# Kernel optimization log

Measured on AMD Instinct MI355X. Metric: run time of the kernel, lower is better.

## Reference

```python
import jax, jax.numpy as jnp
import numpy as np

EMBED_DIM = 1024
NUM_HEADS = 16
RANK = 32
HEAD_DIM = EMBED_DIM // NUM_HEADS
SCALE = 1.0 / np.sqrt(RANK).astype(np.float32)


def setup_inputs() -> dict:
    key = jax.random.key(0)
    ks = jax.random.split(key, 9)
    B, S = 2, 2048
    def lin(k, fan_in, fan_out):
        bound = 1.0 / np.sqrt(fan_in)
        return jax.random.uniform(k, (fan_in, fan_out), jnp.float32, -bound, bound)
    return {
        "hidden_states": jax.random.normal(ks[0], (B, S, EMBED_DIM), jnp.float32),
        "Wq": lin(ks[1], EMBED_DIM, RANK * NUM_HEADS),
        "bq": jnp.zeros((RANK * NUM_HEADS,), jnp.float32),
        "Wk": lin(ks[2], EMBED_DIM, RANK * NUM_HEADS),
        "bk": jnp.zeros((RANK * NUM_HEADS,), jnp.float32),
        "Wv": lin(ks[3], EMBED_DIM, EMBED_DIM),
        "bv": jnp.zeros((EMBED_DIM,), jnp.float32),
        "Wo": lin(ks[4], EMBED_DIM, EMBED_DIM),
        "bo": jnp.zeros((EMBED_DIM,), jnp.float32),
    }


def reference(hidden_states, Wq, bq, Wk, bk, Wv, bv, Wo, bo):
    B, S, E = hidden_states.shape
    q = (hidden_states @ Wq + bq).reshape(B, S, NUM_HEADS, RANK)      # [b,i,h,r]
    k = (hidden_states @ Wk + bk).reshape(B, S, NUM_HEADS, RANK)      # [b,j,h,r]
    v = (hidden_states @ Wv + bv).reshape(B, S, NUM_HEADS, HEAD_DIM)  # [b,j,h,d]
    # full [b,i,j,h] score tensor, softmax over j (axis=2), as in the torch code
    scores = jnp.einsum('bihr,bjhr->bijh', q, k) * SCALE
    attn = jax.nn.softmax(scores, axis=2)
    out = jnp.einsum('bijh,bjhd->bihd', attn, v).reshape(B, S, E)
    return out @ Wo + bo
```

## Files before the change

kernel.cpp:

```cpp
#include <hip/hip_runtime.h>

#define EMBED   1024
#define NHEADS  16
#define RANK    32
#define HDIM    64
#define BATCH   2
#define SEQ     2048
#define BSQ     (BATCH * SEQ)
#define CEXP    0.25505998f

typedef __attribute__((ext_vector_type(8))) short bf16x8;
typedef __attribute__((ext_vector_type(4))) float f32x4;

__device__ __forceinline__ float bf2f(unsigned short u) {
    union { unsigned int i; float f; } x; x.i = ((unsigned int)u) << 16;
    return x.f;
}
__device__ __forceinline__ unsigned short f2bf(float f) {
    union { float f; unsigned int i; } x; x.f = f;
    unsigned int r = x.i + 0x7FFFu + ((x.i >> 16) & 1u);
    return (unsigned short)(r >> 16);
}

#define ASYNC16(gp, lp) \
    __builtin_amdgcn_global_load_lds( \
        (const __attribute__((address_space(1))) void*)(gp), \
        (__attribute__((address_space(3))) void*)(lp), 16, 0, 0)

__global__ __launch_bounds__(256) void prep_all(
    const float* __restrict__ hs,
    const float* __restrict__ Wq, const float* __restrict__ Wk,
    const float* __restrict__ Wv, const float* __restrict__ Wo,
    const float* __restrict__ bq, const float* __restrict__ bk,
    const float* __restrict__ bv,
    unsigned short* __restrict__ hsb, unsigned short* __restrict__ wT_all,
    unsigned short* __restrict__ woT, float* __restrict__ ball)
{
    __shared__ float L[64][65];
    const int blk = blockIdx.x;
    const int t = threadIdx.x;

    if (blk < 2048) {
        const size_t i = ((size_t)blk * 256 + t) * 8;
        float4 v0 = *(const float4*)(hs + i);
        float4 v1 = *(const float4*)(hs + i + 4);
        ushort4 o0, o1;
        o0.x = f2bf(v0.x); o0.y = f2bf(v0.y); o0.z = f2bf(v0.z); o0.w = f2bf(v0.w);
        o1.x = f2bf(v1.x); o1.y = f2bf(v1.y); o1.z = f2bf(v1.z); o1.w = f2bf(v1.w);
        *(ushort4*)(hsb + i) = o0;
        *(ushort4*)(hsb + i + 4) = o1;
        return;
    }
    if (blk < 2816) {
        int idx = blk - 2048;
        int z, bx, by;
        if (idx < 256) { z = idx >> 7; int r2 = idx & 127; bx = r2 & 7; by = r2 >> 3; }
        else { idx -= 256; z = 2 + (idx >> 8); int r2 = idx & 255; bx = r2 & 15; by = r2 >> 4; }
        const int Nw = (z < 2) ? 512 : 1024;
        const float* W = (z == 0) ? Wq : (z == 1) ? Wk : (z == 2) ? Wv : Wo;
        unsigned short* dst = (z == 3) ? woT : (wT_all + (size_t)z * 512 * 1024);

        const int r = t >> 2, c0 = (t & 3) * 16;
        const float* src = W + (size_t)(by * 64 + r) * Nw + bx * 64 + c0;
        #pragma unroll
        for (int u = 0; u < 4; u++)
            *(float4*)&L[r][c0 + 4 * u] = *(const float4*)(src + 4 * u);
        __syncthreads();
        unsigned short* drow = dst + (size_t)(bx * 64 + r) * 1024 + by * 64 + c0;
        #pragma unroll
        for (int u4 = 0; u4 < 4; u4++) {
            ushort4 o;
            o.x = f2bf(L[c0 + 4 * u4 + 0][r]);
            o.y = f2bf(L[c0 + 4 * u4 + 1][r]);
            o.z = f2bf(L[c0 + 4 * u4 + 2][r]);
            o.w = f2bf(L[c0 + 4 * u4 + 3][r]);
            *(ushort4*)(drow + 4 * u4) = o;
        }
        return;
    }
    {
        const int i = (blk - 2816) * 256 + t;
        ball[i] = (i < 512) ? bq[i] : (i < 1024) ? bk[i - 512] : bv[i - 1024];
    }
}

__global__ __launch_bounds__(256) void gemm_qkv(
    const unsigned short* __restrict__ A, const unsigned short* __restrict__ BT,
    const float* __restrict__ bias,
    unsigned short* __restrict__ qH, unsigned short* __restrict__ kH,
    unsigned short* __restrict__ vTout)
{
    __shared__ unsigned short As[128 * 32];
    __shared__ unsigned short Bs[64 * 32];
    const int K = 1024;
    const int t = threadIdx.x;
    const int lane = t & 63;
    const int li = lane & 15, la = lane >> 4;
    const int w = t >> 6;
    const int row0 = blockIdx.y * 128, col0 = blockIdx.x * 64;

    const int sr = lane >> 2, sc2 = (lane & 3) * 8;
    const unsigned short* ag0 = A + (size_t)(row0 + w * 32 + sr) * K + sc2;
    const unsigned short* ag1 = A + (size_t)(row0 + w * 32 + 16 + sr) * K + sc2;
    const unsigned short* bg0 = BT + (size_t)(col0 + w * 16 + sr) * K + sc2;
    unsigned short* lA0 = &As[(w * 32) * 32];
    unsigned short* lA1 = &As[(w * 32 + 16) * 32];
    unsigned short* lB0 = &Bs[(w * 16) * 32];

    f32x4 acc[2][4];
    #pragma unroll
    for (int i = 0; i < 2; i++)
        #pragma unroll
        for (int j = 0; j < 4; j++)
            acc[i][j] = (f32x4){0.f, 0.f, 0.f, 0.f};

    for (int k0 = 0; k0 < K; k0 += 32) {
        ASYNC16(ag0 + k0, lA0);
        ASYNC16(ag1 + k0, lA1);
        ASYNC16(bg0 + k0, lB0);
        __syncthreads();
        bf16x8 af[2], bfr[4];
        #pragma unroll
        for (int mt = 0; mt < 2; mt++)
            af[mt] = *(const bf16x8*)&As[(w * 32 + mt * 16 + li) * 32 + la * 8];
        #pragma unroll
        for (int nt = 0; nt < 4; nt++)
            bfr[nt] = *(const bf16x8*)&Bs[(nt * 16 + li) * 32 + la * 8];
        #pragma unroll
        for (int mt = 0; mt < 2; mt++)
            #pragma unroll
            for (int nt = 0; nt < 4; nt++)
                acc[mt][nt] = __builtin_amdgcn_mfma_f32_16x16x32_bf16(af[mt], bfr[nt], acc[mt][nt], 0, 0, 0);
        __syncthreads();
    }

    const int bb = row0 >> 11;
    const int jb = (row0 & 2047) + w * 32;
    #pragma unroll
    for (int nt = 0; nt < 4; nt++) {
        const int col = col0 + nt * 16 + li;
        const float bval = bias[col];
        if (col < 1024) {
            const int hh = (col & 511) >> 5;
            const int rr = col & 31;
            unsigned short* base = ((col < 512) ? qH : kH)
                + ((size_t)(bb * 16 + hh) * 2048) * 32 + rr;
            #pragma unroll
            for (int mt = 0; mt < 2; mt++)
                #pragma unroll
                for (int r = 0; r < 4; r++)
                    base[(size_t)(jb + mt * 16 + la * 4 + r) * 32] =
                        f2bf(acc[mt][nt][r] + bval);
        } else {
            const int hd = col - 1024;
            unsigned short* dcol = vTout + ((size_t)(bb * 16 + (hd >> 6)) * 64 + (hd & 63)) * SEQ;
            #pragma unroll
            for (int mt = 0; mt < 2; mt++) {
                const int srow = jb + mt * 16 + la * 4;
                ushort4 o;
                o.x = f2bf(acc[mt][nt][0] + bval);
                o.y = f2bf(acc[mt][nt][1] + bval);
                o.z = f2bf(acc[mt][nt][2] + bval);
                o.w = f2bf(acc[mt][nt][3] + bval);
                *(ushort4*)(dcol + srow) = o;
            }
        }
    }
}

__global__ __launch_bounds__(256) void gemm_out(
    const unsigned short* __restrict__ A, const unsigned short* __restrict__ BT,
    const float* __restrict__ bias, float* __restrict__ C)
{
    __shared__ unsigned short As[64 * 32];
    __shared__ unsigned short Bs[64 * 32];
    const int K = 1024;
    const int t = threadIdx.x;
    const int lane = t & 63;
    const int li = lane & 15, la = lane >> 4;
    const int w = t >> 6;
    const int row0 = blockIdx.y * 64, col0 = blockIdx.x * 64;

    const int sr = lane >> 2, sc2 = (lane & 3) * 8;
    const unsigned short* ag0 = A + (size_t)(row0 + w * 16 + sr) * K + sc2;
    const unsigned short* bg0 = BT + (size_t)(col0 + w * 16 + sr) * K + sc2;
    unsigned short* lA0 = &As[(w * 16) * 32];
    unsigned short* lB0 = &Bs[(w * 16) * 32];

    f32x4 acc[4];
    #pragma unroll
    for (int j = 0; j < 4; j++) acc[j] = (f32x4){0.f, 0.f, 0.f, 0.f};

    for (int k0 = 0; k0 < K; k0 += 32) {
        ASYNC16(ag0 + k0, lA0);
        ASYNC16(bg0 + k0, lB0);
        __syncthreads();
        bf16x8 af, bfr[4];
        af = *(const bf16x8*)&As[(w * 16 + li) * 32 + la * 8];
        #pragma unroll
        for (int nt = 0; nt < 4; nt++)
            bfr[nt] = *(const bf16x8*)&Bs[(nt * 16 + li) * 32 + la * 8];
        #pragma unroll
        for (int nt = 0; nt < 4; nt++)
            acc[nt] = __builtin_amdgcn_mfma_f32_16x16x32_bf16(af, bfr[nt], acc[nt], 0, 0, 0);
        __syncthreads();
    }

    #pragma unroll
    for (int nt = 0; nt < 4; nt++) {
        const int col = col0 + nt * 16 + li;
        const float bval = bias[col];
        #pragma unroll
        for (int r = 0; r < 4; r++) {
            const int row = row0 + w * 16 + la * 4 + r;
            C[(size_t)row * 1024 + col] = acc[nt][r] + bval;
        }
    }
}

__global__ __launch_bounds__(256) void attn_v7(
    const unsigned short* __restrict__ qH,
    const unsigned short* __restrict__ kH,
    const unsigned short* __restrict__ vT,
    unsigned short* __restrict__ ao)
{
    __shared__ unsigned short kt[2][64 * 48];
    __shared__ unsigned short vt[2][64 * 72];
    __shared__ unsigned short P[128 * 72];

    const int t = threadIdx.x;
    const int lane = t & 63;
    const int li = lane & 15, la = lane >> 4;
    const int w = t >> 6;

    const int bh = blockIdx.x & 31;
    const int itile = blockIdx.x >> 5;
    const int i0 = itile * 128;
    const int b = bh >> 4, h = bh & 15;

    bf16x8 qf[2];
    #pragma unroll
    for (int it = 0; it < 2; it++) {
        const unsigned short* qp = qH + ((size_t)bh * 2048 + i0 + w * 32 + it * 16 + li) * 32 + la * 8;
        ushort4 q0 = *(const ushort4*)qp;
        ushort4 q1 = *(const ushort4*)(qp + 4);
        short u[8];
        u[0] = (short)f2bf(bf2f(q0.x) * CEXP);
        u[1] = (short)f2bf(bf2f(q0.y) * CEXP);
        u[2] = (short)f2bf(bf2f(q0.z) * CEXP);
        u[3] = (short)f2bf(bf2f(q0.w) * CEXP);
        u[4] = (short)f2bf(bf2f(q1.x) * CEXP);
        u[5] = (short)f2bf(bf2f(q1.y) * CEXP);
        u[6] = (short)f2bf(bf2f(q1.z) * CEXP);
        u[7] = (short)f2bf(bf2f(q1.w) * CEXP);
        qf[it] = *(const bf16x8*)u;
    }

    bf16x8 vones;
    #pragma unroll
    for (int u2 = 0; u2 < 8; u2++) vones[u2] = (short)0x3F80;

    const int kr = t >> 2, kc = (t & 3) * 8;
    const int vr = t >> 3, vc = (t & 7) * 8;
    const unsigned short* kp = kH + (size_t)bh * 2048 * 32 + (size_t)kr * 32 + kc;
    const unsigned short* vp0 = vT + (size_t)bh * 64 * SEQ + (size_t)vr * SEQ + vc;
    const unsigned short* vp1 = vp0 + (size_t)32 * SEQ;

    f32x4 accO[2][4], accl[2];
    #pragma unroll
    for (int mt = 0; mt < 2; mt++) {
        accl[mt] = (f32x4){0.f, 0.f, 0.f, 0.f};
        #pragma unroll
        for (int dt = 0; dt < 4; dt++) accO[mt][dt] = (f32x4){0.f, 0.f, 0.f, 0.f};
    }

    uint4 kreg  = *(const uint4*)(kp);
    uint4 vreg0 = *(const uint4*)(vp0);
    uint4 vreg1 = *(const uint4*)(vp1);
    *(uint4*)&kt[0][kr * 48 + kc] = kreg;
    *(uint4*)&vt[0][vr * 72 + vc] = vreg0;
    *(uint4*)&vt[0][(vr + 32) * 72 + vc] = vreg1;
    kreg  = *(const uint4*)(kp + 64 * 32);
    vreg0 = *(const uint4*)(vp0 + 64);
    vreg1 = *(const uint4*)(vp1 + 64);

    #define ATTN_BODY(BUF, OTHER, JPRE)                                            \
    {                                                                              \
        __syncthreads();                                                           \
        *(uint4*)&kt[OTHER][kr * 48 + kc] = kreg;                                  \
        *(uint4*)&vt[OTHER][vr * 72 + vc] = vreg0;                                 \
        *(uint4*)&vt[OTHER][(vr + 32) * 72 + vc] = vreg1;                          \
        const int jn = (JPRE) & 2047;                                              \
        kreg  = *(const uint4*)(kp + (size_t)jn * 32);                             \
        vreg0 = *(const uint4*)(vp0 + jn);                                         \
        vreg1 = *(const uint4*)(vp1 + jn);                                         \
        f32x4 sc[4][2];                                                            \
        _Pragma("unroll")                                                          \
        for (int jt = 0; jt < 4; jt++) {                                           \
            const bf16x8 kf = *(const bf16x8*)&kt[BUF][(jt * 16 + li) * 48 + la * 8]; \
            sc[jt][0] = __builtin_amdgcn_mfma_f32_16x16x32_bf16(kf, qf[0], (f32x4){0.f,0.f,0.f,0.f}, 0, 0, 0); \
            sc[jt][1] = __builtin_amdgcn_mfma_f32_16x16x32_bf16(kf, qf[1], (f32x4){0.f,0.f,0.f,0.f}, 0, 0, 0); \
        }                                                                          \
        _Pragma("unroll")                                                          \
        for (int jt = 0; jt < 4; jt++)                                             \
            _Pragma("unroll")                                                      \
            for (int it = 0; it < 2; it++) {                                       \
                union { float f; unsigned int u; } c0, c1, c2, c3;                 \
                c0.f = exp2f(sc[jt][it][0]);                                       \
                c1.f = exp2f(sc[jt][it][1]);                                       \
                c2.f = exp2f(sc[jt][it][2]);                                       \
                c3.f = exp2f(sc[jt][it][3]);                                       \
                uint2 pk;                                                          \
                pk.x = __builtin_amdgcn_perm(c1.u + 0x8000u, c0.u + 0x8000u, 0x07060302u); \
                pk.y = __builtin_amdgcn_perm(c3.u + 0x8000u, c2.u + 0x8000u, 0x07060302u); \
                *(uint2*)&P[(w * 32 + it * 16 + li) * 72 + jt * 16 + la * 4] = pk; \
            }                                                                      \
        _Pragma("unroll")                                                          \
        for (int mt = 0; mt < 2; mt++) {                                           \
            _Pragma("unroll")                                                      \
            for (int ks = 0; ks < 2; ks++) {                                       \
                const bf16x8 pf = *(const bf16x8*)&P[(w * 32 + mt * 16 + li) * 72 + ks * 32 + la * 8]; \
                accl[mt] = __builtin_amdgcn_mfma_f32_16x16x32_bf16(pf, vones, accl[mt], 0, 0, 0); \
                _Pragma("unroll")                                                  \
                for (int dt = 0; dt < 4; dt++) {                                   \
                    const bf16x8 vf = *(const bf16x8*)&vt[BUF][(dt * 16 + li) * 72 + ks * 32 + la * 8]; \
                    accO[mt][dt] = __builtin_amdgcn_mfma_f32_16x16x32_bf16(pf, vf, accO[mt][dt], 0, 0, 0); \
                }                                                                  \
            }                                                                      \
        }                                                                          \
    }

    for (int j0 = 0; j0 < SEQ; j0 += 128) {
        ATTN_BODY(0, 1, j0 + 128)
        ATTN_BODY(1, 0, j0 + 192)
    }
    #undef ATTN_BODY

    #pragma unroll
    for (int mt = 0; mt < 2; mt++) {
        float linv[4];
        #pragma unroll
        for (int r = 0; r < 4; r++) linv[r] = 1.f / accl[mt][r];
        #pragma unroll
        for (int dt = 0; dt < 4; dt++)
            #pragma unroll
            for (int r = 0; r < 4; r++) {
                const int row = b * SEQ + i0 + w * 32 + mt * 16 + la * 4 + r;
                ao[(size_t)row * 1024 + h * 64 + dt * 16 + li] = f2bf(accO[mt][dt][r] * linv[r]);
            }
    }
}

extern "C" void kernel_launch(void* const* d_in, const int* in_sizes, int n_in,
                              void* d_out, int out_size, void* d_ws, size_t ws_size,
                              hipStream_t stream) {
    const float* hs = (const float*)d_in[0];
    const float* Wq = (const float*)d_in[1];
    const float* bq = (const float*)d_in[2];
    const float* Wk = (const float*)d_in[3];
    const float* bk = (const float*)d_in[4];
    const float* Wv = (const float*)d_in[5];
    const float* bv = (const float*)d_in[6];
    const float* Wo = (const float*)d_in[7];
    const float* bo = (const float*)d_in[8];

    char* p = (char*)d_ws;
    unsigned short* hsb = (unsigned short*)(p);
    unsigned short* wT  = (unsigned short*)(p + 8388608u);
    unsigned short* woT = (unsigned short*)(p + 12582912u);
    float*          ball= (float*)(p + 14680064u);
    unsigned short* qHb = (unsigned short*)(p + 14688256u);
    unsigned short* kHb = (unsigned short*)(p + 18882560u);
    unsigned short* vTb = (unsigned short*)(p + 23076864u);
    unsigned short* ao  = (unsigned short*)(p + 31465472u);

    prep_all<<<dim3(2824), 256, 0, stream>>>(hs, Wq, Wk, Wv, Wo, bq, bk, bv,
                                             hsb, wT, woT, ball);

    gemm_qkv<<<dim3(32, 32), 256, 0, stream>>>(hsb, wT, ball, qHb, kHb, vTb);

    attn_v7<<<dim3(512), 256, 0, stream>>>(qHb, kHb, vTb, ao);

    gemm_out<<<dim3(16, 64), 256, 0, stream>>>(ao, woT, bo, (float*)d_out);
}
```

Before: 196.2 us.

## Retile QKV and output GEMMs to larger tiles, halve attention query tile

The QKV GEMM moves to 128x128 tiles and the output GEMM to 64x128 tiles, each with a 2x2 warp layout and a 64-wide K step per barrier pair. This raises data reuse per load and halves the number of barriers. The attention kernel drops to 64 query rows per block (16 per warp) and doubles the grid to 1024 blocks, trading per-block K/V reuse for more parallelism and fewer registers. The new GEMM grids have fewer blocks, which may underfill the 256 CUs.

```diff
diff --git a/kernel.cpp b/kernel.cpp
--- a/kernel.cpp
+++ b/kernel.cpp
@@ -90,55 +90,59 @@
     unsigned short* __restrict__ qH, unsigned short* __restrict__ kH,
     unsigned short* __restrict__ vTout)
 {
-    __shared__ unsigned short As[128 * 32];
-    __shared__ unsigned short Bs[64 * 32];
+    __shared__ unsigned short As[2 * 128 * 32];
+    __shared__ unsigned short Bs[2 * 128 * 32];
     const int K = 1024;
     const int t = threadIdx.x;
     const int lane = t & 63;
     const int li = lane & 15, la = lane >> 4;
-    const int w = t >> 6;
-    const int row0 = blockIdx.y * 128, col0 = blockIdx.x * 64;
+    const int w = t >> 6, wm = w >> 1, wn = w & 1;
+    const int row0 = blockIdx.y * 128, col0 = blockIdx.x * 128;
 
     const int sr = lane >> 2, sc2 = (lane & 3) * 8;
-    const unsigned short* ag0 = A + (size_t)(row0 + w * 32 + sr) * K + sc2;
-    const unsigned short* ag1 = A + (size_t)(row0 + w * 32 + 16 + sr) * K + sc2;
-    const unsigned short* bg0 = BT + (size_t)(col0 + w * 16 + sr) * K + sc2;
-    unsigned short* lA0 = &As[(w * 32) * 32];
-    unsigned short* lA1 = &As[(w * 32 + 16) * 32];
-    unsigned short* lB0 = &Bs[(w * 16) * 32];
-
-    f32x4 acc[2][4];
-    #pragma unroll
-    for (int i = 0; i < 2; i++)
+    const unsigned short* ag = A + (size_t)(row0 + sr) * K + sc2;
+    const unsigned short* bg = BT + (size_t)(col0 + sr) * K + sc2;
+
+    f32x4 acc[4][4];
+    #pragma unroll
+    for (int i = 0; i < 4; i++)
         #pragma unroll
         for (int j = 0; j < 4; j++)
             acc[i][j] = (f32x4){0.f, 0.f, 0.f, 0.f};
 
-    for (int k0 = 0; k0 < K; k0 += 32) {
-        ASYNC16(ag0 + k0, lA0);
-        ASYNC16(ag1 + k0, lA1);
-        ASYNC16(bg0 + k0, lB0);
-        __syncthreads();
-        bf16x8 af[2], bfr[4];
-        #pragma unroll
-        for (int mt = 0; mt < 2; mt++)
-            af[mt] = *(const bf16x8*)&As[(w * 32 + mt * 16 + li) * 32 + la * 8];
-        #pragma unroll
-        for (int nt = 0; nt < 4; nt++)
-            bfr[nt] = *(const bf16x8*)&Bs[(nt * 16 + li) * 32 + la * 8];
-        #pragma unroll
-        for (int mt = 0; mt < 2; mt++)
+    for (int k0 = 0; k0 < K; k0 += 64) {
+        #pragma unroll
+        for (int kh = 0; kh < 2; kh++)
+            #pragma unroll
+            for (int u = 0; u < 2; u++) {
+                const int ro = w * 32 + u * 16;
+                ASYNC16(ag + (size_t)ro * K + k0 + kh * 32, &As[kh * 4096 + ro * 32]);
+                ASYNC16(bg + (size_t)ro * K + k0 + kh * 32, &Bs[kh * 4096 + ro * 32]);
+            }
+        __syncthreads();
+        #pragma unroll
+        for (int kh = 0; kh < 2; kh++) {
+            bf16x8 af[4], bfr[4];
+            #pragma unroll
+            for (int mt = 0; mt < 4; mt++)
+                af[mt] = *(const bf16x8*)&As[kh * 4096 + (wm * 64 + mt * 16 + li) * 32 + la * 8];
             #pragma unroll
             for (int nt = 0; nt < 4; nt++)
-                acc[mt][nt] = __builtin_amdgcn_mfma_f32_16x16x32_bf16(af[mt], bfr[nt], acc[mt][nt], 0, 0, 0);
+                bfr[nt] = *(const bf16x8*)&Bs[kh * 4096 + (wn * 64 + nt * 16 + li) * 32 + la * 8];
+            #pragma unroll
+            for (int mt = 0; mt < 4; mt++)
+                #pragma unroll
+                for (int nt = 0; nt < 4; nt++)
+                    acc[mt][nt] = __builtin_amdgcn_mfma_f32_16x16x32_bf16(af[mt], bfr[nt], acc[mt][nt], 0, 0, 0);
+        }
         __syncthreads();
     }
 
     const int bb = row0 >> 11;
-    const int jb = (row0 & 2047) + w * 32;
+    const int jb = (row0 & 2047) + wm * 64;
     #pragma unroll
     for (int nt = 0; nt < 4; nt++) {
-        const int col = col0 + nt * 16 + li;
+        const int col = col0 + wn * 64 + nt * 16 + li;
         const float bval = bias[col];
         if (col < 1024) {
             const int hh = (col & 511) >> 5;
@@ -146,7 +150,7 @@
             unsigned short* base = ((col < 512) ? qH : kH)
                 + ((size_t)(bb * 16 + hh) * 2048) * 32 + rr;
             #pragma unroll
-            for (int mt = 0; mt < 2; mt++)
+            for (int mt = 0; mt < 4; mt++)
                 #pragma unroll
                 for (int r = 0; r < 4; r++)
                     base[(size_t)(jb + mt * 16 + la * 4 + r) * 32] =
@@ -155,7 +159,7 @@
             const int hd = col - 1024;
             unsigned short* dcol = vTout + ((size_t)(bb * 16 + (hd >> 6)) * 64 + (hd & 63)) * SEQ;
             #pragma unroll
-            for (int mt = 0; mt < 2; mt++) {
+            for (int mt = 0; mt < 4; mt++) {
                 const int srow = jb + mt * 16 + la * 4;
                 ushort4 o;
                 o.x = f2bf(acc[mt][nt][0] + bval);
@@ -172,53 +176,70 @@
     const unsigned short* __restrict__ A, const unsigned short* __restrict__ BT,
     const float* __restrict__ bias, float* __restrict__ C)
 {
-    __shared__ unsigned short As[64 * 32];
-    __shared__ unsigned short Bs[64 * 32];
+    __shared__ unsigned short As[2 * 64 * 32];
+    __shared__ unsigned short Bs[2 * 128 * 32];
     const int K = 1024;
     const int t = threadIdx.x;
     const int lane = t & 63;
     const int li = lane & 15, la = lane >> 4;
-    const int w = t >> 6;
-    const int row0 = blockIdx.y * 64, col0 = blockIdx.x * 64;
+    const int w = t >> 6, wm = w >> 1, wn = w & 1;
+    const int row0 = blockIdx.y * 64, col0 = blockIdx.x * 128;
 
     const int sr = lane >> 2, sc2 = (lane & 3) * 8;
-    const unsigned short* ag0 = A + (size_t)(row0 + w * 16 + sr) * K + sc2;
-    const unsigned short* bg0 = BT + (size_t)(col0 + w * 16 + sr) * K + sc2;
-    unsigned short* lA0 = &As[(w * 16) * 32];
-    unsigned short* lB0 = &Bs[(w * 16) * 32];
-
-    f32x4 acc[4];
-    #pragma unroll
-    for (int j = 0; j < 4; j++) acc[j] = (f32x4){0.f, 0.f, 0.f, 0.f};
-
-    for (int k0 = 0; k0 < K; k0 += 32) {
-        ASYNC16(ag0 + k0, lA0);
-        ASYNC16(bg0 + k0, lB0);
-        __syncthreads();
-        bf16x8 af, bfr[4];
-        af = *(const bf16x8*)&As[(w * 16 + li) * 32 + la * 8];
-        #pragma unroll
-        for (int nt = 0; nt < 4; nt++)
-            bfr[nt] = *(const bf16x8*)&Bs[(nt * 16 + li) * 32 + la * 8];
-        #pragma unroll
-        for (int nt = 0; nt < 4; nt++)
-            acc[nt] = __builtin_amdgcn_mfma_f32_16x16x32_bf16(af, bfr[nt], acc[nt], 0, 0, 0);
+    const unsigned short* ag = A + (size_t)(row0 + sr) * K + sc2;
+    const unsigned short* bg = BT + (size_t)(col0 + sr) * K + sc2;
+
+    f32x4 acc[2][4];
+    #pragma unroll
+    for (int i = 0; i < 2; i++)
+        #pragma unroll
+        for (int j = 0; j < 4; j++)
+            acc[i][j] = (f32x4){0.f, 0.f, 0.f, 0.f};
+
+    for (int k0 = 0; k0 < K; k0 += 64) {
+        #pragma unroll
+        for (int kh = 0; kh < 2; kh++) {
+            ASYNC16(ag + (size_t)(w * 16) * K + k0 + kh * 32, &As[kh * 2048 + (w * 16) * 32]);
+            #pragma unroll
+            for (int u = 0; u < 2; u++) {
+                const int ro = w * 32 + u * 16;
+                ASYNC16(bg + (size_t)ro * K + k0 + kh * 32, &Bs[kh * 4096 + ro * 32]);
+            }
+        }
+        __syncthreads();
+        #pragma unroll
+        for (int kh = 0; kh < 2; kh++) {
+            bf16x8 af[2], bfr[4];
+            #pragma unroll
+            for (int mt = 0; mt < 2; mt++)
+                af[mt] = *(const bf16x8*)&As[kh * 2048 + (wm * 32 + mt * 16 + li) * 32 + la * 8];
+            #pragma unroll
+            for (int nt = 0; nt < 4; nt++)
+                bfr[nt] = *(const bf16x8*)&Bs[kh * 4096 + (wn * 64 + nt * 16 + li) * 32 + la * 8];
+            #pragma unroll
+            for (int mt = 0; mt < 2; mt++)
+                #pragma unroll
+                for (int nt = 0; nt < 4; nt++)
+                    acc[mt][nt] = __builtin_amdgcn_mfma_f32_16x16x32_bf16(af[mt], bfr[nt], acc[mt][nt], 0, 0, 0);
+        }
         __syncthreads();
     }
 
     #pragma unroll
     for (int nt = 0; nt < 4; nt++) {
-        const int col = col0 + nt * 16 + li;
+        const int col = col0 + wn * 64 + nt * 16 + li;
         const float bval = bias[col];
         #pragma unroll
-        for (int r = 0; r < 4; r++) {
-            const int row = row0 + w * 16 + la * 4 + r;
-            C[(size_t)row * 1024 + col] = acc[nt][r] + bval;
-        }
-    }
-}
-
-__global__ __launch_bounds__(256) void attn_v7(
+        for (int mt = 0; mt < 2; mt++)
+            #pragma unroll
+            for (int r = 0; r < 4; r++) {
+                const int row = row0 + wm * 32 + mt * 16 + la * 4 + r;
+                C[(size_t)row * 1024 + col] = acc[mt][nt][r] + bval;
+            }
+    }
+}
+
+__global__ __launch_bounds__(256) void attn_v8(
     const unsigned short* __restrict__ qH,
     const unsigned short* __restrict__ kH,
     const unsigned short* __restrict__ vT,
@@ -226,7 +247,7 @@
 {
     __shared__ unsigned short kt[2][64 * 48];
     __shared__ unsigned short vt[2][64 * 72];
-    __shared__ unsigned short P[128 * 72];
+    __shared__ unsigned short P[64 * 72];
 
     const int t = threadIdx.x;
     const int lane = t & 63;
@@ -235,13 +256,12 @@
 
     const int bh = blockIdx.x & 31;
     const int itile = blockIdx.x >> 5;
-    const int i0 = itile * 128;
+    const int i0 = itile * 64;
     const int b = bh >> 4, h = bh & 15;
 
-    bf16x8 qf[2];
-    #pragma unroll
-    for (int it = 0; it < 2; it++) {
-        const unsigned short* qp = qH + ((size_t)bh * 2048 + i0 + w * 32 + it * 16 + li) * 32 + la * 8;
+    bf16x8 qf;
+    {
+        const unsigned short* qp = qH + ((size_t)bh * 2048 + i0 + w * 16 + li) * 32 + la * 8;
         ushort4 q0 = *(const ushort4*)qp;
         ushort4 q1 = *(const ushort4*)(qp + 4);
         short u[8];
@@ -253,7 +273,7 @@
         u[5] = (short)f2bf(bf2f(q1.y) * CEXP);
         u[6] = (short)f2bf(bf2f(q1.z) * CEXP);
         u[7] = (short)f2bf(bf2f(q1.w) * CEXP);
-        qf[it] = *(const bf16x8*)u;
+        qf = *(const bf16x8*)u;
     }
 
     bf16x8 vones;
@@ -266,13 +286,11 @@
     const unsigned short* vp0 = vT + (size_t)bh * 64 * SEQ + (size_t)vr * SEQ + vc;
     const unsigned short* vp1 = vp0 + (size_t)32 * SEQ;
 
-    f32x4 accO[2][4], accl[2];
-    #pragma unroll
-    for (int mt = 0; mt < 2; mt++) {
-        accl[mt] = (f32x4){0.f, 0.f, 0.f, 0.f};
-        #pragma unroll
-        for (int dt = 0; dt < 4; dt++) accO[mt][dt] = (f32x4){0.f, 0.f, 0.f, 0.f};
-    }
+    f32x4 accO[4], accl;
+    accl = (f32x4){0.f, 0.f, 0.f, 0.f};
+    #pragma unroll
+    for (int dt = 0; dt < 4; dt++) accO[dt] = (f32x4){0.f, 0.f, 0.f, 0.f};
+    const int prow = w * 16 + li;
 
     uint4 kreg  = *(const uint4*)(kp);
     uint4 vreg0 = *(const uint4*)(vp0);
@@ -294,38 +312,32 @@
         kreg  = *(const uint4*)(kp + (size_t)jn * 32);                             \
         vreg0 = *(const uint4*)(vp0 + jn);                                         \
         vreg1 = *(const uint4*)(vp1 + jn);                                         \
-        f32x4 sc[4][2];                                                            \
+        f32x4 sc[4];                                                               \
         _Pragma("unroll")                                                          \
         for (int jt = 0; jt < 4; jt++) {                                           \
             const bf16x8 kf = *(const bf16x8*)&kt[BUF][(jt * 16 + li) * 48 + la * 8]; \
-            sc[jt][0] = __builtin_amdgcn_mfma_f32_16x16x32_bf16(kf, qf[0], (f32x4){0.f,0.f,0.f,0.f}, 0, 0, 0); \
-            sc[jt][1] = __builtin_amdgcn_mfma_f32_16x16x32_bf16(kf, qf[1], (f32x4){0.f,0.f,0.f,0.f}, 0, 0, 0); \
+            sc[jt] = __builtin_amdgcn_mfma_f32_16x16x32_bf16(kf, qf, (f32x4){0.f,0.f,0.f,0.f}, 0, 0, 0); \
         }                                                                          \
         _Pragma("unroll")                                                          \
-        for (int jt = 0; jt < 4; jt++)                                             \
+        for (int jt = 0; jt < 4; jt++) {                                           \
+            union { float f; unsigned int u; } c0, c1, c2, c3;                     \
+            c0.f = exp2f(sc[jt][0]);                                               \
+            c1.f = exp2f(sc[jt][1]);                                               \
+            c2.f = exp2f(sc[jt][2]);                                               \
+            c3.f = exp2f(sc[jt][3]);                                               \
+            uint2 pk;                                                              \
+            pk.x = __builtin_amdgcn_perm(c1.u + 0x8000u, c0.u + 0x8000u, 0x07060302u); \
+            pk.y = __builtin_amdgcn_perm(c3.u + 0x8000u, c2.u + 0x8000u, 0x07060302u); \
+            *(uint2*)&P[prow * 72 + jt * 16 + la * 4] = pk;                        \
+        }                                                                          \
+        _Pragma("unroll")                                                          \
+        for (int ks = 0; ks < 2; ks++) {                                           \
+            const bf16x8 pf = *(const bf16x8*)&P[prow * 72 + ks * 32 + la * 8];    \
+            accl = __builtin_amdgcn_mfma_f32_16x16x32_bf16(pf, vones, accl, 0, 0, 0); \
             _Pragma("unroll")                                                      \
-            for (int it = 0; it < 2; it++) {                                       \
-                union { float f; unsigned int u; } c0, c1, c2, c3;                 \
-                c0.f = exp2f(sc[jt][it][0]);                                       \
-                c1.f = exp2f(sc[jt][it][1]);                                       \
-                c2.f = exp2f(sc[jt][it][2]);                                       \
-                c3.f = exp2f(sc[jt][it][3]);                                       \
-                uint2 pk;                                                          \
-                pk.x = __builtin_amdgcn_perm(c1.u + 0x8000u, c0.u + 0x8000u, 0x07060302u); \
-                pk.y = __builtin_amdgcn_perm(c3.u + 0x8000u, c2.u + 0x8000u, 0x07060302u); \
-                *(uint2*)&P[(w * 32 + it * 16 + li) * 72 + jt * 16 + la * 4] = pk; \
-            }                                                                      \
-        _Pragma("unroll")                                                          \
-        for (int mt = 0; mt < 2; mt++) {                                           \
-            _Pragma("unroll")                                                      \
-            for (int ks = 0; ks < 2; ks++) {                                       \
-                const bf16x8 pf = *(const bf16x8*)&P[(w * 32 + mt * 16 + li) * 72 + ks * 32 + la * 8]; \
-                accl[mt] = __builtin_amdgcn_mfma_f32_16x16x32_bf16(pf, vones, accl[mt], 0, 0, 0); \
-                _Pragma("unroll")                                                  \
-                for (int dt = 0; dt < 4; dt++) {                                   \
-                    const bf16x8 vf = *(const bf16x8*)&vt[BUF][(dt * 16 + li) * 72 + ks * 32 + la * 8]; \
-                    accO[mt][dt] = __builtin_amdgcn_mfma_f32_16x16x32_bf16(pf, vf, accO[mt][dt], 0, 0, 0); \
-                }                                                                  \
+            for (int dt = 0; dt < 4; dt++) {                                       \
+                const bf16x8 vf = *(const bf16x8*)&vt[BUF][(dt * 16 + li) * 72 + ks * 32 + la * 8]; \
+                accO[dt] = __builtin_amdgcn_mfma_f32_16x16x32_bf16(pf, vf, accO[dt], 0, 0, 0); \
             }                                                                      \
         }                                                                          \
     }
@@ -336,19 +348,16 @@
     }
     #undef ATTN_BODY
 
-    #pragma unroll
-    for (int mt = 0; mt < 2; mt++) {
-        float linv[4];
-        #pragma unroll
-        for (int r = 0; r < 4; r++) linv[r] = 1.f / accl[mt][r];
-        #pragma unroll
-        for (int dt = 0; dt < 4; dt++)
-            #pragma unroll
-            for (int r = 0; r < 4; r++) {
-                const int row = b * SEQ + i0 + w * 32 + mt * 16 + la * 4 + r;
-                ao[(size_t)row * 1024 + h * 64 + dt * 16 + li] = f2bf(accO[mt][dt][r] * linv[r]);
-            }
-    }
+    float linv[4];
+    #pragma unroll
+    for (int r = 0; r < 4; r++) linv[r] = 1.f / accl[r];
+    #pragma unroll
+    for (int dt = 0; dt < 4; dt++)
+        #pragma unroll
+        for (int r = 0; r < 4; r++) {
+            const int row = b * SEQ + i0 + w * 16 + la * 4 + r;
+            ao[(size_t)row * 1024 + h * 64 + dt * 16 + li] = f2bf(accO[dt][r] * linv[r]);
+        }
 }
 
 extern "C" void kernel_launch(void* const* d_in, const int* in_sizes, int n_in,
@@ -377,9 +386,9 @@
     prep_all<<<dim3(2824), 256, 0, stream>>>(hs, Wq, Wk, Wv, Wo, bq, bk, bv,
                                              hsb, wT, woT, ball);
 
-    gemm_qkv<<<dim3(32, 32), 256, 0, stream>>>(hsb, wT, ball, qHb, kHb, vTb);
-
-    attn_v7<<<dim3(512), 256, 0, stream>>>(qHb, kHb, vTb, ao);
-
-    gemm_out<<<dim3(16, 64), 256, 0, stream>>>(ao, woT, bo, (float*)d_out);
-}
+    gemm_qkv<<<dim3(16, 32), 256, 0, stream>>>(hsb, wT, ball, qHb, kHb, vTb);
+
+    attn_v8<<<dim3(1024), 256, 0, stream>>>(qHb, kHb, vTb, ao);
+
+    gemm_out<<<dim3(8, 64), 256, 0, stream>>>(ao, woT, bo, (float*)d_out);
+}
```

Result: faster. 189.5 us (-3.4%).
